# Optimization experiments

Hardware: AMD Instinct MI355X
Metric: run time of the kernel (lower is better)

## Reference

```python
import jax, jax.numpy as jnp
import numpy as np

B, C, H, W = 2, 3, 512, 512
P = 16
D = 768
NH = 12
DEPTH = 12
MLP = 4
HP, WP = H // P, W // P
N = HP * WP
DH = D // NH          # 64
ROPE_BASE = 100.0     # from pos_embed='RoPE100'


def _ln(x, w, b, eps):
    m = jnp.mean(x, -1, keepdims=True)
    v = jnp.mean((x - m) ** 2, -1, keepdims=True)
    return (x - m) * jax.lax.rsqrt(v + eps) * w + b


def _rope_tables(maxpos, d):
    inv = 1.0 / (ROPE_BASE ** (jnp.arange(0, d, 2, dtype=jnp.float32) / d))
    f = jnp.arange(maxpos, dtype=jnp.float32)[:, None] * inv[None, :]
    f = jnp.concatenate([f, f], -1)  # [maxpos, d]
    return jnp.cos(f), jnp.sin(f)


def _rot_half(x):
    x1, x2 = jnp.split(x, 2, -1)
    return jnp.concatenate([-x2, x1], -1)


def _rope2d(t, pos, cos, sin):
    # t: [B,NH,N,DH]; pos: [B,N,2] (y,x). First half of DH rotated by y, second by x.
    def rot1d(tok, p):
        c = cos[p][:, None]  # [B,1,N,DH//2]
        s = sin[p][:, None]
        return tok * c + _rot_half(tok) * s
    ty, tx = jnp.split(t, 2, -1)
    return jnp.concatenate([rot1d(ty, pos[..., 0]), rot1d(tx, pos[..., 1])], -1)


def _forward(image, patch_w, patch_b, ln1_w, ln1_b, qkv_w, qkv_b, proj_w, proj_b,
             ln2_w, ln2_b, fc1_w, fc1_b, fc2_w, fc2_b, encn_w, encn_b):
    # patch embed: conv stride=patch, flatten row-major (y-major, matching cartesian_prod(y,x))
    x = jax.lax.conv_general_dilated(image, patch_w, (P, P), 'VALID',
                                     dimension_numbers=('NCHW', 'OIHW', 'NCHW'))
    x = (x + patch_b[None, :, None, None]).reshape(B, D, N).transpose(0, 2, 1)  # [B,N,D]
    yy, xx = jnp.meshgrid(jnp.arange(HP), jnp.arange(WP), indexing='ij')
    pos = jnp.broadcast_to(jnp.stack([yy, xx], -1).reshape(N, 2), (B, N, 2))
    cos, sin = _rope_tables(max(HP, WP), DH // 2)
    scale = DH ** -0.5
    for i in range(DEPTH):
        h = _ln(x, ln1_w[i], ln1_b[i], 1e-5)
        qkv = (h @ qkv_w[i].T + qkv_b[i]).reshape(B, N, 3, NH, DH).transpose(2, 0, 3, 1, 4)
        q, k, v = qkv[0], qkv[1], qkv[2]  # [B,NH,N,DH]
        q = _rope2d(q, pos, cos, sin)
        k = _rope2d(k, pos, cos, sin)
        att = jax.nn.softmax(jnp.einsum('bhqd,bhkd->bhqk', q, k) * scale, -1)
        o = jnp.einsum('bhqk,bhkd->bhqd', att, v).transpose(0, 2, 1, 3).reshape(B, N, D)
        x = x + o @ proj_w[i].T + proj_b[i]
        h = _ln(x, ln2_w[i], ln2_b[i], 1e-5)
        h = jax.nn.gelu(h @ fc1_w[i].T + fc1_b[i], approximate=False)
        x = x + h @ fc2_w[i].T + fc2_b[i]
    x = _ln(x, encn_w, encn_b, 1e-6)
    return x, pos


def setup_inputs() -> dict:
    key = jax.random.key(0)
    ks = jax.random.split(key, 8)
    s = 0.02
    dff = MLP * D
    return {
        "image": jax.random.normal(ks[0], (B, C, H, W), jnp.float32),
        "true_shape": jnp.full((B, 2), H, jnp.int32),
        "patch_w": jax.random.normal(ks[1], (D, C, P, P), jnp.float32) * s,
        "patch_b": jnp.zeros((D,), jnp.float32),
        "ln1_w": jnp.ones((DEPTH, D), jnp.float32),
        "ln1_b": jnp.zeros((DEPTH, D), jnp.float32),
        "qkv_w": jax.random.normal(ks[2], (DEPTH, 3 * D, D), jnp.float32) * s,
        "qkv_b": jnp.zeros((DEPTH, 3 * D), jnp.float32),
        "proj_w": jax.random.normal(ks[3], (DEPTH, D, D), jnp.float32) * s,
        "proj_b": jnp.zeros((DEPTH, D), jnp.float32),
        "ln2_w": jnp.ones((DEPTH, D), jnp.float32),
        "ln2_b": jnp.zeros((DEPTH, D), jnp.float32),
        "fc1_w": jax.random.normal(ks[4], (DEPTH, dff, D), jnp.float32) * s,
        "fc1_b": jnp.zeros((DEPTH, dff), jnp.float32),
        "fc2_w": jax.random.normal(ks[5], (DEPTH, D, dff), jnp.float32) * s,
        "fc2_b": jnp.zeros((DEPTH, D), jnp.float32),
        "encn_w": jnp.ones((D,), jnp.float32),
        "encn_b": jnp.zeros((D,), jnp.float32),
    }


def reference(image, true_shape, patch_w, patch_b, ln1_w, ln1_b, qkv_w, qkv_b,
              proj_w, proj_b, ln2_w, ln2_b, fc1_w, fc1_b, fc2_w, fc2_b,
              encn_w, encn_b):
    # true_shape assumed full-resolution (all images H x W); positions are static grid
    return _forward(image, patch_w, patch_b, ln1_w, ln1_b, qkv_w, qkv_b, proj_w,
                    proj_b, ln2_w, ln2_b, fc1_w, fc1_b, fc2_w, fc2_b, encn_w, encn_b)
```

## Files before the change

kernel.cpp:

```cpp
#include <hip/hip_runtime.h>
#include <hip/hip_bf16.h>
#include <stdint.h>

typedef unsigned short u16;
typedef __attribute__((ext_vector_type(8))) short bf16x8;
typedef __attribute__((ext_vector_type(4))) float f32x4;
typedef __attribute__((ext_vector_type(4))) u16 u16x4;
typedef __attribute__((ext_vector_type(4))) uint32_t u32x4;

__device__ __forceinline__ u16 f2bf(float f) {
  union { float f; uint32_t u; } v; v.f = f;
  uint32_t u = v.u + 0x7FFFu + ((v.u >> 16) & 1u);
  return (u16)(u >> 16);
}
__device__ __forceinline__ float bf2f(u16 h) {
  union { uint32_t u; float f; } v; v.u = ((uint32_t)h) << 16;
  return v.f;
}

__device__ __forceinline__ int xcd_swz(int hw, int n) {
  return (n & 7) ? hw : (hw & 7) * (n >> 3) + (hw >> 3);
}

__device__ __forceinline__ void gload_lds16(const void* g, void* l) {
  __builtin_amdgcn_global_load_lds(
      (const __attribute__((address_space(1))) void*)g,
      (__attribute__((address_space(3))) void*)l, 16, 0, 0);
}

__global__ __launch_bounds__(256) void cast_f32_bf16(const float* __restrict__ src,
                                                     u16* __restrict__ dst, int n4) {
  int i = blockIdx.x * 256 + threadIdx.x;
  if (i < n4) {
    float4 v = ((const float4*)src)[i];
    u16x4 o; o.x = f2bf(v.x); o.y = f2bf(v.y); o.z = f2bf(v.z); o.w = f2bf(v.w);
    ((u16x4*)dst)[i] = o;
  }
}

__global__ __launch_bounds__(256) void im2col_kernel(const float* __restrict__ img,
                                                     u16* __restrict__ out) {
  int f = blockIdx.x * 256 + threadIdx.x;
  int row = blockIdx.y;
  int b = row >> 10, n = row & 1023, py = n >> 5, px = n & 31;
  int c = f >> 8, rem = f & 255, i = rem >> 4, j = rem & 15;
  float v = img[(((size_t)b * 3 + c) * 512 + py * 16 + i) * 512 + px * 16 + j];
  out[(size_t)row * 768 + f] = f2bf(v);
}

template <int EPI, int XGX, int XGY, int XGZ>
__global__ __launch_bounds__(256, 2)
void gemm_bt(const u16* __restrict__ A, const u16* __restrict__ W,
             const float* __restrict__ bias, void* __restrict__ outp,
             int M, int N, int K, int lda, int ldw) {
  constexpr int AB = 128 * 128;
  constexpr int BB = 128 * 128;
  constexpr int BUF = AB + BB;
  constexpr int LOADS = BUF / 4096;
  __shared__ char smem[2 * BUF];
  const int tid = threadIdx.x;
  const int lane = tid & 63;
  const int w = tid >> 6;
  const int qr = lane & 15;
  const int kg = lane >> 4;
  const int gx = gridDim.x, gy = gridDim.y;
  const int hw = blockIdx.x + gx * (blockIdx.y + gy * blockIdx.z);
  const int xcd = hw & 7, i = hw >> 3;
  const int sx = gx / XGX, sy = gy / XGY;
  const int cx = xcd % XGX, cy = (xcd / XGX) % XGY, cz = xcd / (XGX * XGY);
  const int bn = cx * sx + i % sx;
  const int rr_ = i / sx;
  const int bm = cy * sy + rr_ % sy;
  const int bz = cz * (gridDim.z / XGZ) + rr_ / sy;
  const int wr = (w >> 1) * 64;
  const int wc = (w & 1) * 64;
  const size_t arow0 = (size_t)bm * 128;
  const size_t wrow0 = (size_t)bn * 128;
  const u16* Ab = A + (size_t)bz * K;
  const u16* Wb = W + (size_t)bz * K;

  f32x4 acc[4][4] = {};

  auto stage = [&](int buf, int kt) {
    char* As = smem + buf * BUF;
    char* Ws = As + AB;
#pragma unroll
    for (int r = 0; r < 4; ++r) {
      int o = r * 4096 + tid * 16;
      int row = o >> 7;
      int lc = (o & 127) ^ ((row & 7) << 4);
      gload_lds16(Ab + (arow0 + row) * lda + kt + (lc >> 1), As + o);
    }
#pragma unroll
    for (int r = 0; r < 4; ++r) {
      int o = r * 4096 + tid * 16;
      int row = o >> 7;
      int lc = (o & 127) ^ ((row & 7) << 4);
      gload_lds16(Wb + (wrow0 + row) * ldw + kt + (lc >> 1), Ws + o);
    }
  };

  const int nt = K >> 6;
  stage(0, 0);
  stage(1, 64);
  for (int t = 0; t < nt; ++t) {
    if (t + 1 < nt) {
      asm volatile("s_waitcnt vmcnt(%0)" :: "i"(LOADS) : "memory");
    } else {
      asm volatile("s_waitcnt vmcnt(0)" ::: "memory");
    }
    __builtin_amdgcn_s_barrier();
    const char* As = smem + (t & 1) * BUF;
    const char* Ws = As + AB;
    bf16x8 af[2][4], bfr[2][4];
#pragma unroll
    for (int m = 0; m < 4; ++m) {
      int row = wr + m * 16 + qr;
      af[0][m] = *(const bf16x8*)(As + row * 128 + ((kg * 16) ^ ((row & 7) << 4)));
    }
#pragma unroll
    for (int n = 0; n < 4; ++n) {
      int row = wc + n * 16 + qr;
      bfr[0][n] = *(const bf16x8*)(Ws + row * 128 + ((kg * 16) ^ ((row & 7) << 4)));
    }
    __builtin_amdgcn_sched_barrier(0);
#pragma unroll
    for (int m = 0; m < 4; ++m) {
      int row = wr + m * 16 + qr;
      af[1][m] = *(const bf16x8*)(As + row * 128 + ((64 + kg * 16) ^ ((row & 7) << 4)));
    }
#pragma unroll
    for (int n = 0; n < 4; ++n) {
      int row = wc + n * 16 + qr;
      bfr[1][n] = *(const bf16x8*)(Ws + row * 128 + ((64 + kg * 16) ^ ((row & 7) << 4)));
    }
    asm volatile("s_waitcnt lgkmcnt(8)" ::: "memory");
    __builtin_amdgcn_sched_barrier(0);
#pragma unroll
    for (int m = 0; m < 4; ++m)
#pragma unroll
      for (int n = 0; n < 4; ++n)
        acc[m][n] = __builtin_amdgcn_mfma_f32_16x16x32_bf16(af[0][m], bfr[0][n], acc[m][n], 0, 0, 0);
    asm volatile("s_waitcnt lgkmcnt(0)" ::: "memory");
    __builtin_amdgcn_sched_barrier(0);
    __builtin_amdgcn_s_barrier();
    if (t + 2 < nt) stage(t & 1, (t + 2) << 6);
#pragma unroll
    for (int m = 0; m < 4; ++m)
#pragma unroll
      for (int n = 0; n < 4; ++n)
        acc[m][n] = __builtin_amdgcn_mfma_f32_16x16x32_bf16(af[1][m], bfr[1][n], acc[m][n], 0, 0, 0);
  }

  const int r0 = bm * 128 + wr + kg * 4;
  const int c0 = bn * 128 + wc + qr;
  if constexpr (EPI == 4) {
    const int headbase = bn * 128 + wc;
    const bool isqk = headbase < 1536;
    const float linv = exp2f(-0.41524101186092122f * (float)qr);
    u16* outb = (u16*)outp;
#pragma unroll
    for (int m = 0; m < 4; ++m) {
#pragma unroll
      for (int j = 0; j < 4; ++j) {
        int row = r0 + m * 16 + j;
        int tok = row & 1023;
        float vs[4];
#pragma unroll
        for (int n = 0; n < 4; ++n) vs[n] = acc[m][n][j] + bias[c0 + n * 16];
        if (isqk) {
          float sy, cy, sxv, cxv;
          __sincosf((float)(tok >> 5) * linv, &sy, &cy);
          __sincosf((float)(tok & 31) * linv, &sxv, &cxv);
          float a0 = vs[0], a1 = vs[1], a2 = vs[2], a3 = vs[3];
          vs[0] = a0 * cy - a1 * sy;
          vs[1] = a1 * cy + a0 * sy;
          vs[2] = a2 * cxv - a3 * sxv;
          vs[3] = a3 * cxv + a2 * sxv;
        }
#pragma unroll
        for (int n = 0; n < 4; ++n)
          outb[(size_t)row * N + c0 + n * 16] = f2bf(vs[n]);
      }
    }
  } else if constexpr (EPI == 5) {
    u16* outb = (u16*)outp + (size_t)bz * M * N;
#pragma unroll
    for (int m = 0; m < 4; ++m)
#pragma unroll
      for (int j = 0; j < 4; ++j) {
        int row = r0 + m * 16 + j;
#pragma unroll
        for (int n = 0; n < 4; ++n)
          outb[(size_t)row * N + c0 + n * 16] = f2bf(acc[m][n][j]);
      }
  } else {
    u16* outb = (u16*)outp;
#pragma unroll
    for (int m = 0; m < 4; ++m)
#pragma unroll
      for (int j = 0; j < 4; ++j) {
        int row = r0 + m * 16 + j;
#pragma unroll
        for (int n = 0; n < 4; ++n) {
          int col = c0 + n * 16;
          float v = acc[m][n][j] + bias[col];
          v = 0.5f * v * (1.0f + erff(v * 0.70710678118654752f));
          outb[(size_t)row * N + col] = f2bf(v);
        }
      }
  }
}

template <int FINAL>
__global__ __launch_bounds__(192)
void fuse_red_ln(const u16* __restrict__ parts, const float* __restrict__ bias,
                 const u16* __restrict__ resid, u16* __restrict__ xout,
                 void* __restrict__ lnout, const float* __restrict__ lw,
                 const float* __restrict__ lb, float eps) {
  if (FINAL && blockIdx.x >= 2048) {
    int i = (blockIdx.x - 2048) * 192 + threadIdx.x;
    if (i < 4096) {
      int c = i & 1, n = (i >> 1) & 1023;
      ((float*)lnout)[(size_t)2048 * 768 + i] = (float)(c ? (n & 31) : (n >> 5));
    }
    return;
  }
  const int row = blockIdx.x, t = threadIdx.x;
  const int c0 = t * 4;
  constexpr size_t MN = (size_t)2048 * 768;
  const u16x4 pa = *(const u16x4*)(parts + (size_t)row * 768 + c0);
  const u16x4 pb = *(const u16x4*)(parts + MN + (size_t)row * 768 + c0);
  const f32x4 bi = *(const f32x4*)(bias + c0);
  f32x4 v;
#pragma unroll
  for (int j = 0; j < 4; ++j) v[j] = bf2f(pa[j]) + bf2f(pb[j]) + bi[j];
  if (resid) {
    const u16x4 rv = *(const u16x4*)(resid + (size_t)row * 768 + c0);
#pragma unroll
    for (int j = 0; j < 4; ++j) v[j] += bf2f(rv[j]);
  }
  if (xout) {
    u16x4 xo;
#pragma unroll
    for (int j = 0; j < 4; ++j) xo[j] = f2bf(v[j]);
    *(u16x4*)(xout + (size_t)row * 768 + c0) = xo;
#pragma unroll
    for (int j = 0; j < 4; ++j) v[j] = bf2f(xo[j]);
  }
  float s = (v[0] + v[1]) + (v[2] + v[3]);
  float sq = (v[0] * v[0] + v[1] * v[1]) + (v[2] * v[2] + v[3] * v[3]);
#pragma unroll
  for (int m = 1; m < 64; m <<= 1) {
    s += __shfl_xor(s, m);
    sq += __shfl_xor(sq, m);
  }
  __shared__ float red[6];
  int wv = t >> 6;
  if ((t & 63) == 0) { red[wv] = s; red[3 + wv] = sq; }
  __syncthreads();
  s = red[0] + red[1] + red[2];
  sq = red[3] + red[4] + red[5];
  float mean = s * (1.0f / 768.0f);
  float var = sq * (1.0f / 768.0f) - mean * mean;
  float rstd = rsqrtf(var + eps);
  const f32x4 lwv = *(const f32x4*)(lw + c0);
  const f32x4 lbv = *(const f32x4*)(lb + c0);
  if (FINAL) {
    f32x4 o;
#pragma unroll
    for (int j = 0; j < 4; ++j) o[j] = (v[j] - mean) * rstd * lwv[j] + lbv[j];
    *(f32x4*)((float*)lnout + (size_t)row * 768 + c0) = o;
  } else {
    u16x4 o;
#pragma unroll
    for (int j = 0; j < 4; ++j) o[j] = f2bf((v[j] - mean) * rstd * lwv[j] + lbv[j]);
    *(u16x4*)((u16*)lnout + (size_t)row * 768 + c0) = o;
  }
}

__global__ __launch_bounds__(128)
void attn_kernel(const u16* __restrict__ qkv, u16* __restrict__ o) {
  __shared__ char smem[32768];
  const int tid = threadIdx.x, lane = tid & 63, w = tid >> 6;
  const int qr = lane & 15, kg = lane >> 4;
  const bool kgodd = (kg & 1) != 0;
  const int lid = xcd_swz(blockIdx.x, gridDim.x);
  const int qb = lid & 31, bh = lid >> 5;
  const int b = bh / 12, h = bh % 12;
  const int qrow0 = qb * 32 + w * 16;
  const u16* kvb = qkv + (size_t)b * 1024 * 2304;

  bf16x8 aq[2];
  {
    const u16* qbase = qkv + ((size_t)(b * 1024 + qrow0 + qr)) * 2304 + h * 64;
    aq[0] = *(const bf16x8*)(qbase + kg * 8);
    aq[1] = *(const bf16x8*)(qbase + 32 + kg * 8);
#pragma unroll
    for (int r = 0; r < 2; ++r)
#pragma unroll
      for (int e = 0; e < 8; ++e)
        aq[r][e] = (short)f2bf(bf2f((u16)aq[r][e]) * 0.125f);
  }
  f32x4 oacc[4] = {};
  float lsum = 0.f;

  const int kvp = tid >> 3, dg = tid & 7;
  bf16x8 va[2], vb[2];
  auto issueV = [&](int kt) {
#pragma unroll
    for (int rr = 0; rr < 2; ++rr) {
      int p = rr * 16 + kvp;
      const u16* vsrc = kvb + ((size_t)(kt * 64 + 2 * p)) * 2304 + 1536 + h * 64 + dg * 8;
      va[rr] = *(const bf16x8*)vsrc;
      vb[rr] = *(const bf16x8*)(vsrc + 2304);
    }
  };
  auto issueK = [&](int kt, int bsel) {
    char* Ks = smem + bsel * 8192;
#pragma unroll
    for (int r = 0; r < 4; ++r) {
      int off = r * 2048 + tid * 16;
      int kv = off >> 7;
      int db = (off ^ ((kv & 7) << 4)) & 127;
      gload_lds16(kvb + ((size_t)(kt * 64 + kv)) * 2304 + 768 + h * 64 + (db >> 1), Ks + off);
    }
  };
  auto writeV = [&](int bsel) {
    char* Vt = smem + 16384 + bsel * 8192;
#pragma unroll
    for (int rr = 0; rr < 2; ++rr) {
      int p = rr * 16 + kvp;
#pragma unroll
      for (int j = 0; j < 8; ++j) {
        int d = dg * 8 + j;
        uint32_t pk = (uint32_t)(u16)va[rr][j] | ((uint32_t)(u16)vb[rr][j] << 16);
        *(uint32_t*)(Vt + ((d * 128 + p * 4) ^ (((dg ^ j) & 7) << 4))) = pk;
      }
    }
  };

  issueV(0);
  issueK(0, 0);
  writeV(0);

  for (int kt = 0; kt < 16; ++kt) {
    const int c = kt & 1;
    asm volatile("s_waitcnt vmcnt(0) lgkmcnt(0)" ::: "memory");
    __builtin_amdgcn_s_barrier();
    if (kt + 1 < 16) { issueV(kt + 1); issueK(kt + 1, c ^ 1); }

    const char* Ks = smem + c * 8192;
    const char* Vt = smem + 16384 + c * 8192;

    bf16x8 bk[2][4];
#pragma unroll
    for (int n = 0; n < 4; ++n) {
      int row = n * 16 + qr;
      bk[0][n] = *(const bf16x8*)(Ks + ((row * 128 + kg * 16) ^ ((row & 7) << 4)));
    }
    __builtin_amdgcn_sched_barrier(0);
#pragma unroll
    for (int n = 0; n < 4; ++n) {
      int row = n * 16 + qr;
      bk[1][n] = *(const bf16x8*)(Ks + ((row * 128 + 64 + kg * 16) ^ ((row & 7) << 4)));
    }
    f32x4 sa[4] = {};
    asm volatile("s_waitcnt lgkmcnt(4)" ::: "memory");
    __builtin_amdgcn_sched_barrier(0);
    __builtin_amdgcn_s_setprio(1);
#pragma unroll
    for (int n = 0; n < 4; ++n)
      sa[n] = __builtin_amdgcn_mfma_f32_16x16x32_bf16(bk[0][n], aq[0], sa[n], 0, 0, 0);
    asm volatile("s_waitcnt lgkmcnt(0)" ::: "memory");
    __builtin_amdgcn_sched_barrier(0);
#pragma unroll
    for (int n = 0; n < 4; ++n)
      sa[n] = __builtin_amdgcn_mfma_f32_16x16x32_bf16(bk[1][n], aq[1], sa[n], 0, 0, 0);
    __builtin_amdgcn_s_setprio(0);

    float pv[4][4];
    float ts = 0.f;
#pragma unroll
    for (int n = 0; n < 4; ++n)
#pragma unroll
      for (int j = 0; j < 4; ++j) {
        pv[n][j] = __expf(sa[n][j]);
        ts += pv[n][j];
      }
    lsum += ts;

    if (kt + 1 < 16) writeV(c ^ 1);

    bf16x8 vf[2][4];
#pragma unroll
    for (int ks = 0; ks < 2; ++ks)
#pragma unroll
      for (int n = 0; n < 4; ++n) {
        int d = n * 16 + qr;
        vf[ks][n] = *(const bf16x8*)(Vt + ((d * 128 + ks * 64 + kg * 16) ^ ((((d >> 3) ^ (d & 7)) & 7) << 4)));
      }

    uint32_t pk0[4], pk1[4];
#pragma unroll
    for (int n = 0; n < 4; ++n) {
      asm("v_cvt_pk_bf16_f32 %0, %1, %2" : "=v"(pk0[n]) : "v"(pv[n][0]), "v"(pv[n][1]));
      asm("v_cvt_pk_bf16_f32 %0, %1, %2" : "=v"(pk1[n]) : "v"(pv[n][2]), "v"(pv[n][3]));
    }
    bf16x8 pb[2];
#pragma unroll
    for (int ks = 0; ks < 2; ++ks) {
      uint32_t A0 = pk0[ks * 2], B0 = pk0[ks * 2 + 1];
      uint32_t A1 = pk1[ks * 2], B1 = pk1[ks * 2 + 1];
      asm("v_permlane32_swap_b32 %0, %1" : "+v"(A0), "+v"(B0));
      asm("v_permlane32_swap_b32 %0, %1" : "+v"(A1), "+v"(B1));
      uint32_t sA0 = (uint32_t)__shfl_xor((int)A0, 16);
      uint32_t sA1 = (uint32_t)__shfl_xor((int)A1, 16);
      uint32_t sB0 = (uint32_t)__shfl_xor((int)B0, 16);
      uint32_t sB1 = (uint32_t)__shfl_xor((int)B1, 16);
      u32x4 dd;
      dd.x = kgodd ? sB0 : A0;
      dd.y = kgodd ? sB1 : A1;
      dd.z = kgodd ? B0 : sA0;
      dd.w = kgodd ? B1 : sA1;
      pb[ks] = __builtin_bit_cast(bf16x8, dd);
    }

    __builtin_amdgcn_s_setprio(1);
#pragma unroll
    for (int ks = 0; ks < 2; ++ks)
#pragma unroll
      for (int n = 0; n < 4; ++n)
        oacc[n] = __builtin_amdgcn_mfma_f32_16x16x32_bf16(vf[ks][n], pb[ks], oacc[n], 0, 0, 0);
    __builtin_amdgcn_s_setprio(0);
  }
  lsum += __shfl_xor(lsum, 16);
  lsum += __shfl_xor(lsum, 32);
  float inv = 1.0f / lsum;
  const size_t rowg = (size_t)(b * 1024 + qrow0 + qr);
#pragma unroll
  for (int n = 0; n < 4; ++n) {
    u16x4 ov;
#pragma unroll
    for (int j = 0; j < 4; ++j) ov[j] = f2bf(oacc[n][j] * inv);
    *(u16x4*)(o + rowg * 768 + h * 64 + n * 16 + kg * 4) = ov;
  }
}

extern "C" void kernel_launch(void* const* d_in, const int* in_sizes, int n_in,
                              void* d_out, int out_size, void* d_ws, size_t ws_size,
                              hipStream_t stream) {
  const float* image  = (const float*)d_in[0];
  const float* patch_w = (const float*)d_in[2];
  const float* patch_b = (const float*)d_in[3];
  const float* ln1_w = (const float*)d_in[4];
  const float* ln1_b = (const float*)d_in[5];
  const float* qkv_w = (const float*)d_in[6];
  const float* qkv_b = (const float*)d_in[7];
  const float* proj_w = (const float*)d_in[8];
  const float* proj_b = (const float*)d_in[9];
  const float* ln2_w = (const float*)d_in[10];
  const float* ln2_b = (const float*)d_in[11];
  const float* fc1_w = (const float*)d_in[12];
  const float* fc1_b = (const float*)d_in[13];
  const float* fc2_w = (const float*)d_in[14];
  const float* fc2_b = (const float*)d_in[15];
  const float* encn_w = (const float*)d_in[16];
  const float* encn_b = (const float*)d_in[17];

  char* ws = (char*)d_ws;
  size_t off = 0;
  auto alloc = [&](size_t bytes) {
    char* pr = ws + off;
    off += (bytes + 255) & ~(size_t)255;
    return pr;
  };

  u16* x      = (u16*)alloc((size_t)2048 * 768 * 2);
  u16* hbuf   = (u16*)alloc((size_t)2048 * 768 * 2);
  u16* qkvb   = (u16*)alloc((size_t)2048 * 2304 * 2);
  u16* obuf   = (u16*)alloc((size_t)2048 * 768 * 2);
  u16* h2     = (u16*)alloc((size_t)2048 * 3072 * 2);
  u16* wpb    = (u16*)alloc((size_t)768 * 768 * 2);
  u16* parts  = (u16*)alloc((size_t)2 * 2048 * 768 * 2);

  const size_t wq_n = (size_t)12 * 2304 * 768;
  const size_t wp_n = (size_t)12 * 768 * 768;
  const size_t w1_n = (size_t)12 * 3072 * 768;
  const size_t w2_n = (size_t)12 * 3072 * 768;
  bool upfront = (off + 2 * (wq_n + wp_n + w1_n + w2_n) + (1u << 20)) <= ws_size;

  u16 *wq, *wp, *w1, *w2;
  if (upfront) {
    wq = (u16*)alloc(wq_n * 2);
    wp = (u16*)alloc(wp_n * 2);
    w1 = (u16*)alloc(w1_n * 2);
    w2 = (u16*)alloc(w2_n * 2);
  } else {
    wq = (u16*)alloc((size_t)2304 * 768 * 2);
    wp = (u16*)alloc((size_t)768 * 768 * 2);
    w1 = (u16*)alloc((size_t)3072 * 768 * 2);
    w2 = (u16*)alloc((size_t)3072 * 768 * 2);
  }

  auto cast = [&](const float* s, u16* d, size_t n) {
    int n4 = (int)(n / 4);
    cast_f32_bf16<<<(n4 + 255) / 256, 256, 0, stream>>>(s, d, n4);
  };

  cast(patch_w, wpb, (size_t)768 * 768);
  if (upfront) {
    cast(qkv_w, wq, wq_n);
    cast(proj_w, wp, wp_n);
    cast(fc1_w, w1, w1_n);
    cast(fc2_w, w2, w2_n);
  }

  im2col_kernel<<<dim3(3, 2048), 256, 0, stream>>>(image, hbuf);
  gemm_bt<5, 2, 2, 2><<<dim3(6, 16, 2), 256, 0, stream>>>(hbuf, wpb, nullptr, parts, 2048, 768, 384, 768, 768);
  fuse_red_ln<0><<<2048, 192, 0, stream>>>(parts, patch_b, nullptr, x, hbuf, ln1_w, ln1_b, 1e-5f);

  for (int L = 0; L < 12; ++L) {
    u16 *wqL, *wpL, *w1L, *w2L;
    if (upfront) {
      wqL = wq + (size_t)L * 2304 * 768;
      wpL = wp + (size_t)L * 768 * 768;
      w1L = w1 + (size_t)L * 3072 * 768;
      w2L = w2 + (size_t)L * 3072 * 768;
    } else {
      cast(qkv_w + (size_t)L * 2304 * 768, wq, (size_t)2304 * 768);
      cast(proj_w + (size_t)L * 768 * 768, wp, (size_t)768 * 768);
      cast(fc1_w + (size_t)L * 3072 * 768, w1, (size_t)3072 * 768);
      cast(fc2_w + (size_t)L * 768 * 3072, w2, (size_t)3072 * 768);
      wqL = wq; wpL = wp; w1L = w1; w2L = w2;
    }
    gemm_bt<4, 2, 4, 1><<<dim3(18, 16), 256, 0, stream>>>(hbuf, wqL, qkv_b + L * 2304, qkvb, 2048, 2304, 768, 768, 768);
    attn_kernel<<<768, 128, 0, stream>>>(qkvb, obuf);
    gemm_bt<5, 2, 2, 2><<<dim3(6, 16, 2), 256, 0, stream>>>(obuf, wpL, nullptr, parts, 2048, 768, 384, 768, 768);
    fuse_red_ln<0><<<2048, 192, 0, stream>>>(parts, proj_b + L * 768, x, x, hbuf,
                                             ln2_w + L * 768, ln2_b + L * 768, 1e-5f);
    gemm_bt<1, 2, 4, 1><<<dim3(24, 16), 256, 0, stream>>>(hbuf, w1L, fc1_b + L * 3072, h2, 2048, 3072, 768, 768, 768);
    gemm_bt<5, 2, 2, 2><<<dim3(6, 16, 2), 256, 0, stream>>>(h2, w2L, nullptr, parts, 2048, 768, 1536, 3072, 3072);
    if (L < 11) {
      fuse_red_ln<0><<<2048, 192, 0, stream>>>(parts, fc2_b + L * 768, x, x, hbuf,
                                               ln1_w + (L + 1) * 768, ln1_b + (L + 1) * 768, 1e-5f);
    } else {
      fuse_red_ln<1><<<2070, 192, 0, stream>>>(parts, fc2_b + L * 768, x, nullptr, (float*)d_out,
                                               encn_w, encn_b, 1e-6f);
    }
  }
}
```

Before: 1.245 ms.

## Split attention over two KV halves with combine kernel; merge weight casts

The attention kernel now splits the 16 KV tiles into two halves, doubling the grid to 1536 blocks. Each block writes an unnormalized bf16 partial output and its row sum, and a new combine kernel adds the two halves and normalizes. The intent is more parallelism and occupancy for attention. The cost is an extra launch and extra global traffic for the partials, plus an added bf16 rounding step on them. The five upfront weight casts are also merged into one launch to cut launch overhead.

```diff
diff --git a/kernel.cpp b/kernel.cpp
--- a/kernel.cpp
+++ b/kernel.cpp
@@ -36,6 +36,26 @@
     u16x4 o; o.x = f2bf(v.x); o.y = f2bf(v.y); o.z = f2bf(v.z); o.w = f2bf(v.w);
     ((u16x4*)dst)[i] = o;
   }
+}
+
+__global__ __launch_bounds__(256)
+void cast_all(const float* __restrict__ s0, const float* __restrict__ s1,
+              const float* __restrict__ s2, const float* __restrict__ s3,
+              const float* __restrict__ s4,
+              u16* __restrict__ d0, u16* __restrict__ d1, u16* __restrict__ d2,
+              u16* __restrict__ d3, u16* __restrict__ d4,
+              long n0, long n1, long n2, long n3, long n4) {
+  long i = (long)blockIdx.x * 256 + threadIdx.x;
+  const float* s; u16* d; long off;
+  if (i < n0) { s = s0; d = d0; off = i; }
+  else if (i < n0 + n1) { s = s1; d = d1; off = i - n0; }
+  else if (i < n0 + n1 + n2) { s = s2; d = d2; off = i - n0 - n1; }
+  else if (i < n0 + n1 + n2 + n3) { s = s3; d = d3; off = i - n0 - n1 - n2; }
+  else if (i < n0 + n1 + n2 + n3 + n4) { s = s4; d = d4; off = i - n0 - n1 - n2 - n3; }
+  else return;
+  float4 v = ((const float4*)s)[off];
+  u16x4 o; o.x = f2bf(v.x); o.y = f2bf(v.y); o.z = f2bf(v.z); o.w = f2bf(v.w);
+  ((u16x4*)d)[off] = o;
 }
 
 __global__ __launch_bounds__(256) void im2col_kernel(const float* __restrict__ img,
@@ -280,15 +300,16 @@
 }
 
 __global__ __launch_bounds__(128)
-void attn_kernel(const u16* __restrict__ qkv, u16* __restrict__ o) {
+void attn_kernel(const u16* __restrict__ qkv, u16* __restrict__ po, float* __restrict__ pl) {
   __shared__ char smem[32768];
   const int tid = threadIdx.x, lane = tid & 63, w = tid >> 6;
   const int qr = lane & 15, kg = lane >> 4;
   const bool kgodd = (kg & 1) != 0;
   const int lid = xcd_swz(blockIdx.x, gridDim.x);
-  const int qb = lid & 31, bh = lid >> 5;
+  const int kvh = lid & 1, qb = (lid >> 1) & 31, bh = lid >> 6;
   const int b = bh / 12, h = bh % 12;
   const int qrow0 = qb * 32 + w * 16;
+  const int kt0 = kvh * 8, kt1 = kt0 + 8;
   const u16* kvb = qkv + (size_t)b * 1024 * 2304;
 
   bf16x8 aq[2];
@@ -340,15 +361,15 @@
     }
   };
 
-  issueV(0);
-  issueK(0, 0);
+  issueV(kt0);
+  issueK(kt0, 0);
   writeV(0);
 
-  for (int kt = 0; kt < 16; ++kt) {
+  for (int kt = kt0; kt < kt1; ++kt) {
     const int c = kt & 1;
     asm volatile("s_waitcnt vmcnt(0) lgkmcnt(0)" ::: "memory");
     __builtin_amdgcn_s_barrier();
-    if (kt + 1 < 16) { issueV(kt + 1); issueK(kt + 1, c ^ 1); }
+    if (kt + 1 < kt1) { issueV(kt + 1); issueK(kt + 1, c ^ 1); }
 
     const char* Ks = smem + c * 8192;
     const char* Vt = smem + 16384 + c * 8192;
@@ -390,7 +411,7 @@
       }
     lsum += ts;
 
-    if (kt + 1 < 16) writeV(c ^ 1);
+    if (kt + 1 < kt1) writeV(c ^ 1);
 
     bf16x8 vf[2][4];
 #pragma unroll
@@ -436,15 +457,32 @@
   }
   lsum += __shfl_xor(lsum, 16);
   lsum += __shfl_xor(lsum, 32);
-  float inv = 1.0f / lsum;
   const size_t rowg = (size_t)(b * 1024 + qrow0 + qr);
+  u16* pob = po + (size_t)kvh * 2048 * 768;
 #pragma unroll
   for (int n = 0; n < 4; ++n) {
     u16x4 ov;
 #pragma unroll
-    for (int j = 0; j < 4; ++j) ov[j] = f2bf(oacc[n][j] * inv);
-    *(u16x4*)(o + rowg * 768 + h * 64 + n * 16 + kg * 4) = ov;
-  }
+    for (int j = 0; j < 4; ++j) ov[j] = f2bf(oacc[n][j]);
+    *(u16x4*)(pob + rowg * 768 + h * 64 + n * 16 + kg * 4) = ov;
+  }
+  if (kg == 0) pl[(size_t)kvh * 2048 * 12 + rowg * 12 + h] = lsum;
+}
+
+__global__ __launch_bounds__(256)
+void attn_combine(const u16* __restrict__ po, const float* __restrict__ pl,
+                  u16* __restrict__ o) {
+  int i = blockIdx.x * 256 + threadIdx.x;
+  int row = i / 192, rc = i - row * 192;
+  int c0 = rc * 4, h = c0 >> 6;
+  constexpr size_t MN = (size_t)2048 * 768;
+  u16x4 a = *(const u16x4*)(po + (size_t)row * 768 + c0);
+  u16x4 bq = *(const u16x4*)(po + MN + (size_t)row * 768 + c0);
+  float inv = 1.0f / (pl[row * 12 + h] + pl[2048 * 12 + row * 12 + h]);
+  u16x4 ov;
+#pragma unroll
+  for (int j = 0; j < 4; ++j) ov[j] = f2bf((bf2f(a[j]) + bf2f(bq[j])) * inv);
+  *(u16x4*)(o + (size_t)row * 768 + c0) = ov;
 }
 
 extern "C" void kernel_launch(void* const* d_in, const int* in_sizes, int n_in,
@@ -483,6 +521,7 @@
   u16* h2     = (u16*)alloc((size_t)2048 * 3072 * 2);
   u16* wpb    = (u16*)alloc((size_t)768 * 768 * 2);
   u16* parts  = (u16*)alloc((size_t)2 * 2048 * 768 * 2);
+  float* lparts = (float*)alloc((size_t)2 * 2048 * 12 * 4);
 
   const size_t wq_n = (size_t)12 * 2304 * 768;
   const size_t wp_n = (size_t)12 * 768 * 768;
@@ -508,12 +547,15 @@
     cast_f32_bf16<<<(n4 + 255) / 256, 256, 0, stream>>>(s, d, n4);
   };
 
-  cast(patch_w, wpb, (size_t)768 * 768);
   if (upfront) {
-    cast(qkv_w, wq, wq_n);
-    cast(proj_w, wp, wp_n);
-    cast(fc1_w, w1, w1_n);
-    cast(fc2_w, w2, w2_n);
+    long n0 = (long)(wq_n / 4), n1 = (long)(wp_n / 4), n2 = (long)(w1_n / 4),
+         n3 = (long)(w2_n / 4), n4 = (long)(768 * 768 / 4);
+    long ntot = n0 + n1 + n2 + n3 + n4;
+    cast_all<<<(int)((ntot + 255) / 256), 256, 0, stream>>>(
+        qkv_w, proj_w, fc1_w, fc2_w, patch_w, wq, wp, w1, w2, wpb,
+        n0, n1, n2, n3, n4);
+  } else {
+    cast(patch_w, wpb, (size_t)768 * 768);
   }
 
   im2col_kernel<<<dim3(3, 2048), 256, 0, stream>>>(image, hbuf);
@@ -535,7 +577,8 @@
       wqL = wq; wpL = wp; w1L = w1; w2L = w2;
     }
     gemm_bt<4, 2, 4, 1><<<dim3(18, 16), 256, 0, stream>>>(hbuf, wqL, qkv_b + L * 2304, qkvb, 2048, 2304, 768, 768, 768);
-    attn_kernel<<<768, 128, 0, stream>>>(qkvb, obuf);
+    attn_kernel<<<1536, 128, 0, stream>>>(qkvb, parts, lparts);
+    attn_combine<<<1536, 256, 0, stream>>>(parts, lparts, obuf);
     gemm_bt<5, 2, 2, 2><<<dim3(6, 16, 2), 256, 0, stream>>>(obuf, wpL, nullptr, parts, 2048, 768, 384, 768, 768);
     fuse_red_ln<0><<<2048, 192, 0, stream>>>(parts, proj_b + L * 768, x, x, hbuf,
                                              ln2_w + L * 768, ln2_b + L * 768, 1e-5f);
```

Result: slower. 1.334 ms (+7.2%).
